# Kernel optimization log

Measured on AMD Instinct MI355X. Metric: run time of the kernel, lower is better.

## Reference

```python
import jax, jax.numpy as jnp
import numpy as np

B_GRAPHS = 64
N_PER = 2048          # nodes per graph (uniform -> total = B*N)
D = 256               # hidden_dim
U = D // 2            # GRU units per direction
L_LAYERS = 2


def setup_inputs() -> dict:
    key = jax.random.key(0)
    ks = jax.random.split(key, 8)
    T = B_GRAPHS * N_PER
    states = jax.random.normal(ks[0], (T, D), dtype=jnp.float32)
    rng = np.random.default_rng(0)
    pos = np.zeros((B_GRAPHS, N_PER), dtype=np.int32)
    for g in range(B_GRAPHS):
        mask = rng.random(N_PER) < 0.5
        L = int(mask.sum())
        pos[g, mask] = rng.permutation(L).astype(np.int32) + 1
    node_positions = jnp.asarray(pos.reshape(-1))
    graph_sizes = jnp.full((B_GRAPHS,), N_PER, dtype=jnp.int32)
    # GRU params (Keras GRU reset_after=True): kernel [D,3u], recurrent [u,3u], bias [2,3u]
    def mk(k):
        k1, k2, k3 = jax.random.split(k, 3)
        K = jax.random.normal(k1, (L_LAYERS, D, 3 * U), dtype=jnp.float32) * 0.06
        R = jax.random.normal(k2, (L_LAYERS, U, 3 * U), dtype=jnp.float32) * 0.06
        b = jax.random.normal(k3, (L_LAYERS, 2, 3 * U), dtype=jnp.float32) * 0.02
        return K, R, b
    K_fwd, R_fwd, b_fwd = mk(ks[1])
    K_bwd, R_bwd, b_bwd = mk(ks[2])
    return {"states": states, "node_positions": node_positions,
            "graph_sizes": graph_sizes, "training": 0,
            "K_fwd": K_fwd, "R_fwd": R_fwd, "b_fwd": b_fwd,
            "K_bwd": K_bwd, "R_bwd": R_bwd, "b_bwd": b_bwd}


def _gru_dir(seq, mask, K, R, b, reverse):
    # seq [B,S,Din], mask [B,S] -> outputs [B,S,U] (Keras GRU, reset_after=True)
    xs = jnp.swapaxes(seq, 0, 1)                 # [S,B,Din]
    ms = jnp.swapaxes(mask, 0, 1)                # [S,B]
    x_proj = xs @ K + b[0]                       # [S,B,3U] input projections
    Bsz = seq.shape[0]
    h0 = jnp.zeros((Bsz, U), seq.dtype)
    def step(h, inp):
        xp, m = inp
        hp = h @ R + b[1]                        # [B,3U]
        xz, xr, xh = jnp.split(xp, 3, axis=-1)
        hz, hr, hh = jnp.split(hp, 3, axis=-1)
        z = jax.nn.sigmoid(xz + hz)
        r = jax.nn.sigmoid(xr + hr)
        cand = jnp.tanh(xh + r * hh)
        h_new = z * h + (1.0 - z) * cand
        h = jnp.where(m[:, None], h_new, h)      # padded steps carry state
        return h, h
    _, ys = jax.lax.scan(step, h0, (x_proj, ms), reverse=reverse)
    return jnp.swapaxes(ys, 0, 1)


def _forward(states, node_positions, graph_sizes, training,
             K_fwd, R_fwd, b_fwd, K_bwd, R_bwd, b_bwd):
    T = states.shape[0]
    B = graph_sizes.shape[0]
    S = T // B  # max leaf-seq length (uniform graph sizes; bounds leaf count)
    gid = jnp.repeat(jnp.arange(B, dtype=jnp.int32), graph_sizes,
                     total_repeat_length=T)                      # [T]
    leaf = node_positions != 0                                   # [T]
    pos0 = node_positions - 1                                    # valid where leaf
    slot = jnp.where(leaf, pos0, S)                              # dump non-leaves
    # Pack ragged leaf sequences into dense [B,S,D] (extra slot S = trash)
    seq = jnp.zeros((B, S + 1, D), states.dtype).at[gid, slot].set(states)[:, :S]
    smask = jnp.zeros((B, S + 1), bool).at[gid, slot].set(leaf)[:, :S]
    drop_rate = 0.1 * float(training)
    x = seq
    key = jax.random.key(42)
    for l in range(L_LAYERS):
        yf = _gru_dir(x, smask, K_fwd[l], R_fwd[l], b_fwd[l], reverse=False)
        yb = _gru_dir(x, smask, K_bwd[l], R_bwd[l], b_bwd[l], reverse=True)
        x = jnp.concatenate([yf, yb], axis=-1)                   # [B,S,D]
        if drop_rate > 0.0:
            key, sub = jax.random.split(key)
            keep = jax.random.bernoulli(sub, 1.0 - drop_rate, x.shape)
            x = jnp.where(keep, x / (1.0 - drop_rate), 0.0)
    # Unpack: leaf nodes get RNN output, non-leaves keep original state
    gathered = x[gid, jnp.clip(pos0, 0)]                         # [T,D]
    return jnp.where(leaf[:, None], gathered, states)


def reference(states, node_positions, graph_sizes, training,
              K_fwd, R_fwd, b_fwd, K_bwd, R_bwd, b_bwd):
    return _forward(states, node_positions, graph_sizes, training,
                    K_fwd, R_fwd, b_fwd, K_bwd, R_bwd, b_bwd)
```

## Files before the change

kernel.cpp:

```cpp
#include <hip/hip_runtime.h>
#include <hip/hip_bf16.h>

#define B_GRAPHS 64
#define NPER     2048
#define T_NODES  (B_GRAPHS*NPER)
#define D_DIM    256
#define U_DIM    128
#define TU       384
#define XPW      768

typedef unsigned short ushortT;
typedef unsigned int   uint32;

typedef __attribute__((ext_vector_type(4))) float  f32x4;
typedef __attribute__((ext_vector_type(8))) __bf16 bf16x8;
typedef _Float16 f16;
typedef __attribute__((ext_vector_type(2))) _Float16 f16x2;

static __device__ __forceinline__ ushortT f2bf(float f) {
  union { float f; uint32 u; } a; a.f = f;
  uint32 u = a.u;
  return (ushortT)((u + 0x7fffu + ((u >> 16) & 1u)) >> 16);
}
static __device__ __forceinline__ float bf2f(ushortT h) {
  union { uint32 u; float f; } a; a.u = ((uint32)h) << 16; return a.f;
}
static __device__ __forceinline__ f16x2 u2h(uint32 u) {
  union { uint32 u; f16x2 h; } x; x.u = u; return x.h;
}
static __device__ __forceinline__ float dot2f(f16x2 a, f16x2 b, float c) {
#if __has_builtin(__builtin_amdgcn_fdot2)
  return __builtin_amdgcn_fdot2(a, b, c, false);
#else
  return c + (float)a.x * (float)b.x + (float)a.y * (float)b.y;
#endif
}

__global__ __launch_bounds__(256) void prep_kernel(
    const float* __restrict__ Kf, const float* __restrict__ Kb,
    const float* __restrict__ bfw, const float* __restrict__ bbw,
    ushortT* __restrict__ Wt, float* __restrict__ b0)
{
  int idx = blockIdx.x * 256 + threadIdx.x;
  if (idx < 2 * XPW * D_DIM) {
    int l = idx / (XPW * D_DIM);
    int rem = idx % (XPW * D_DIM);
    int c = rem / D_DIM, k = rem % D_DIM;
    float v = (c < TU) ? Kf[(size_t)l * D_DIM * TU + (size_t)k * TU + c]
                       : Kb[(size_t)l * D_DIM * TU + (size_t)k * TU + (c - TU)];
    Wt[idx] = f2bf(v);
  } else {
    int i2 = idx - 2 * XPW * D_DIM;
    if (i2 < 2 * XPW) {
      int l = i2 / XPW, c = i2 % XPW;
      b0[i2] = (c < TU) ? bfw[l * 2 * TU + c] : bbw[l * 2 * TU + (c - TU)];
    }
  }
}

__global__ __launch_bounds__(256) void nodeofL_kernel(
    const int* __restrict__ pos, int* __restrict__ nodeof, int* __restrict__ L)
{
  int g = blockIdx.x, tid = threadIdx.x;
  __shared__ int red[256];
  int cnt = 0;
  for (int i = 0; i < NPER / 256; ++i) {
    int t = g * NPER + i * 256 + tid;
    int p = pos[t];
    if (p) { nodeof[g * NPER + p - 1] = t; cnt++; }
  }
  red[tid] = cnt; __syncthreads();
  for (int s = 128; s > 0; s >>= 1) {
    if (tid < s) red[tid] += red[tid + s];
    __syncthreads();
  }
  if (tid == 0) L[g] = red[0];
}

#if __has_builtin(__builtin_amdgcn_global_load_lds)
#define GLD_LDS(gsrc, ldst) \
  __builtin_amdgcn_global_load_lds((const __attribute__((address_space(1))) void*)(gsrc), \
                                   (__attribute__((address_space(3))) void*)(ldst), 16, 0, 0)
#define HAVE_GLD_LDS 1
#else
#define HAVE_GLD_LDS 0
#endif

__global__ __launch_bounds__(256) void gemm_kernel(
    const float* __restrict__ statesA, const ushortT* __restrict__ Adense,
    const ushortT* __restrict__ Wt, const float* __restrict__ b0,
    const int* __restrict__ nodeof, const int* __restrict__ L,
    ushortT* __restrict__ xp, int layer, int mode)
{
  int mblk = blockIdx.x, nblk = blockIdx.y;
  int g = mblk >> 4;
  int sBase = (mblk & 15) << 7;
  int Lg = L[g];
  if (sBase >= Lg) return;

  __shared__ __align__(16) ushortT As[128 * 32];
  __shared__ __align__(16) ushortT Bs[128 * 32];

  int tid = threadIdx.x;
  int lane = tid & 63, wid = tid >> 6;
  int wr = wid >> 1, wc = wid & 1;
  f32x4 acc[4][4];
  for (int i = 0; i < 4; i++) for (int n = 0; n < 4; n++) acc[i][n] = (f32x4){0.f,0.f,0.f,0.f};

  for (int kb = 0; kb < 8; ++kb) {
    __syncthreads();
    for (int c = 0; c < 2; ++c) {
      int flat = c * 4096 + tid * 16;
      int col = flat >> 6;
      size_t srcB = ((size_t)(layer * XPW + nblk * 128 + col)) * 512 + kb * 64 + (flat & 63);
#if HAVE_GLD_LDS
      GLD_LDS((const char*)Wt + srcB, (char*)Bs + c * 4096 + wid * 1024);
#else
      *(uint4*)((char*)Bs + flat) = *(const uint4*)((const char*)Wt + srcB);
#endif
    }
    if (mode) {
      for (int c = 0; c < 2; ++c) {
        int flat = c * 4096 + tid * 16;
        int row = flat >> 6;
        size_t srcA = ((size_t)(mblk * 128 + row)) * 512 + kb * 64 + (flat & 63);
#if HAVE_GLD_LDS
        GLD_LDS((const char*)Adense + srcA, (char*)As + c * 4096 + wid * 1024);
#else
        *(uint4*)((char*)As + flat) = *(const uint4*)((const char*)Adense + srcA);
#endif
      }
    } else {
      for (int c = 0; c < 2; ++c) {
        int flat = c * 4096 + tid * 16;
        int row = flat >> 6;
        int s = sBase + row;
        if (s < Lg) {
          int nt = nodeof[g * NPER + s];
          const float* sp = statesA + (size_t)nt * D_DIM + kb * 32 + ((flat & 63) >> 1);
          float4 u0 = *(const float4*)sp;
          float4 u1 = *(const float4*)(sp + 4);
          union { ushortT us[8]; uint4 v; } pk;
          pk.us[0] = f2bf(u0.x); pk.us[1] = f2bf(u0.y); pk.us[2] = f2bf(u0.z); pk.us[3] = f2bf(u0.w);
          pk.us[4] = f2bf(u1.x); pk.us[5] = f2bf(u1.y); pk.us[6] = f2bf(u1.z); pk.us[7] = f2bf(u1.w);
          *(uint4*)((char*)As + flat) = pk.v;
        }
      }
    }
    __syncthreads();

    bf16x8 af[4], bfr[4];
    for (int i = 0; i < 4; i++) {
      int off = (wr * 64 + i * 16 + (lane & 15)) * 32 + (lane >> 4) * 8;
      af[i] = *(const bf16x8*)&As[off];
    }
    for (int n = 0; n < 4; n++) {
      int off = (wc * 64 + n * 16 + (lane & 15)) * 32 + (lane >> 4) * 8;
      bfr[n] = *(const bf16x8*)&Bs[off];
    }
    for (int i = 0; i < 4; i++)
      for (int n = 0; n < 4; n++)
        acc[i][n] = __builtin_amdgcn_mfma_f32_16x16x32_bf16(af[i], bfr[n], acc[i][n], 0, 0, 0);
  }

  for (int n = 0; n < 4; n++) {
    int gcol = nblk * 128 + wc * 64 + n * 16 + (lane & 15);
    float bb = b0[layer * XPW + gcol];
    for (int i = 0; i < 4; i++) {
      int rowBase = mblk * 128 + wr * 64 + i * 16 + (lane >> 4) * 4;
      for (int v = 0; v < 4; v++)
        xp[(size_t)(rowBase + v) * XPW + gcol] = f2bf(acc[i][n][v] + bb);
    }
  }
}

__global__ __launch_bounds__(768) void rec_kernel(
    const ushortT* __restrict__ xp,
    const float* __restrict__ Rf, const float* __restrict__ Rb,
    const float* __restrict__ bfw, const float* __restrict__ bbw,
    const int* __restrict__ L, ushortT* __restrict__ y, int layer)
{
  int g = blockIdx.x, dir = blockIdx.y;
  int Lg = L[g];
  if (Lg == 0) return;
  int tid = threadIdx.x;
  int col = tid % TU;
  int khalf = tid / TU;

  __shared__ __align__(16) f16 hpk[128];
  __shared__ float hp[768];

  const float* R = (dir ? Rb : Rf) + (size_t)layer * U_DIM * TU;
  f16x2 rr[32];
  #pragma unroll
  for (int m = 0; m < 32; ++m) {
    int k = khalf * 64 + 2 * m;
    f16x2 p;
    p.x = (f16)R[(size_t)k * TU + col];
    p.y = (f16)R[(size_t)(k + 1) * TU + col];
    rr[m] = p;
  }
  float b1col = (dir ? bbw : bfw)[layer * 2 * TU + TU + col];
  float accInit = khalf ? 0.0f : b1col;

  if (tid < 128) hpk[tid] = (f16)0.0f;
  float hreg = 0.0f;
  __syncthreads();

  int j = tid;
  ushortT xzu = 0, xru = 0, xhu = 0;
  size_t xbase = (size_t)g * NPER * XPW + (size_t)dir * TU;
  if (tid < 128) {
    int pos = dir ? (Lg - 1) : 0;
    const ushortT* p = xp + xbase + (size_t)pos * XPW + j;
    xzu = p[0]; xru = p[128]; xhu = p[256];
  }

  for (int s = 0; s < Lg; ++s) {
    float a0 = accInit, a1 = 0.0f;
    const uint4* hv = (const uint4*)&hpk[khalf * 64];
    #pragma unroll
    for (int m4 = 0; m4 < 8; ++m4) {
      uint4 q = hv[m4];
      a0 = dot2f(u2h(q.x), rr[4 * m4 + 0], a0);
      a1 = dot2f(u2h(q.y), rr[4 * m4 + 1], a1);
      a0 = dot2f(u2h(q.z), rr[4 * m4 + 2], a0);
      a1 = dot2f(u2h(q.w), rr[4 * m4 + 3], a1);
    }
    hp[tid] = a0 + a1;
    __syncthreads();

    if (tid < 128) {
      int pos = dir ? (Lg - 1 - s) : s;
      float hz = hp[j]       + hp[TU + j];
      float hr = hp[128 + j] + hp[TU + 128 + j];
      float hh = hp[256 + j] + hp[TU + 256 + j];
      float xz = bf2f(xzu), xr = bf2f(xru), xh = bf2f(xhu);
      float z = 1.0f / (1.0f + __expf(-(xz + hz)));
      float r = 1.0f / (1.0f + __expf(-(xr + hr)));
      float ch = xh + r * hh;
      float e = __expf(2.0f * fabsf(ch));
      float th = 1.0f - 2.0f / (e + 1.0f);
      float cand = (ch >= 0.0f) ? th : -th;
      float hnew = z * hreg + (1.0f - z) * cand;
      hreg = hnew;
      hpk[j] = (f16)hnew;
      y[(size_t)(g * NPER + pos) * D_DIM + dir * U_DIM + j] = f2bf(hnew);
      int s2 = s + 1;
      if (s2 < Lg) {
        int pos2 = dir ? (Lg - 1 - s2) : s2;
        const ushortT* p = xp + xbase + (size_t)pos2 * XPW + j;
        xzu = p[0]; xru = p[128]; xhu = p[256];
      }
    }
    __syncthreads();
  }
}

__global__ __launch_bounds__(256) void unpack_kernel(
    const float* __restrict__ states, const int* __restrict__ pos,
    const ushortT* __restrict__ y, float* __restrict__ out)
{
  int node = blockIdx.x * 4 + (threadIdx.x >> 6);
  int lane = threadIdx.x & 63;
  int p = pos[node];
  int g = node >> 11;
  float4 v;
  if (p) {
    const ushortT* yp = y + (size_t)(g * NPER + p - 1) * D_DIM + lane * 4;
    v = make_float4(bf2f(yp[0]), bf2f(yp[1]), bf2f(yp[2]), bf2f(yp[3]));
  } else {
    v = *(const float4*)(states + (size_t)node * D_DIM + lane * 4);
  }
  *(float4*)(out + (size_t)node * D_DIM + lane * 4) = v;
}

extern "C" void kernel_launch(void* const* d_in, const int* in_sizes, int n_in,
                              void* d_out, int out_size, void* d_ws, size_t ws_size,
                              hipStream_t stream) {
  const float* states = (const float*)d_in[0];
  const int*   pos    = (const int*)d_in[1];
  const float* Kf  = (const float*)d_in[4];
  const float* Rf  = (const float*)d_in[5];
  const float* bfw = (const float*)d_in[6];
  const float* Kb  = (const float*)d_in[7];
  const float* Rb  = (const float*)d_in[8];
  const float* bbw = (const float*)d_in[9];

  char* ws = (char*)d_ws;
  int*     L      = (int*)(ws + 0);
  int*     nodeof = (int*)(ws + 256);
  ushortT* Wt     = (ushortT*)(ws + 524544);
  float*   b0     = (float*)(ws + 1310976);
  ushortT* xp     = (ushortT*)(ws + 1317120);
  ushortT* y      = (ushortT*)(ws + 202643712);

  prep_kernel<<<1542, 256, 0, stream>>>(Kf, Kb, bfw, bbw, Wt, b0);
  nodeofL_kernel<<<64, 256, 0, stream>>>(pos, nodeof, L);

  dim3 ggrid(1024, 6);
  dim3 rgrid(64, 2);

  gemm_kernel<<<ggrid, 256, 0, stream>>>(states, (const ushortT*)nullptr, Wt, b0, nodeof, L, xp, 0, 0);
  rec_kernel<<<rgrid, 768, 0, stream>>>(xp, Rf, Rb, bfw, bbw, L, y, 0);
  gemm_kernel<<<ggrid, 256, 0, stream>>>(states, y, Wt, b0, nodeof, L, xp, 1, 1);
  rec_kernel<<<rgrid, 768, 0, stream>>>(xp, Rf, Rb, bfw, bbw, L, y, 1);

  unpack_kernel<<<32768, 256, 0, stream>>>(states, pos, y, (float*)d_out);
}
```

Before: 1.529 ms.

## Restructure GRU recurrence to one barrier per step with double-buffered hidden state

The recurrent kernel drops from 768 to 256 threads. Each lane now computes all three gates for one unit over half of K, and the two halves are combined with a cross-lane shuffle instead of a shared-memory partial-sum array. The hidden state is double-buffered in LDS, so each step needs only one barrier instead of two. The xp inputs are prefetched two steps ahead, and divisions use hardware reciprocals. The gains come from a shorter serial critical path per time step, at the cost of three times more register-held weights per thread (96 packed f16 pairs) and slightly lower-precision reciprocals.

```diff
diff --git a/kernel.cpp b/kernel.cpp
--- a/kernel.cpp
+++ b/kernel.cpp
@@ -33,6 +33,13 @@
   return __builtin_amdgcn_fdot2(a, b, c, false);
 #else
   return c + (float)a.x * (float)b.x + (float)a.y * (float)b.y;
+#endif
+}
+static __device__ __forceinline__ float rcpf(float x) {
+#if __has_builtin(__builtin_amdgcn_rcpf)
+  return __builtin_amdgcn_rcpf(x);
+#else
+  return 1.0f / x;
 #endif
 }
 
@@ -174,7 +181,7 @@
   }
 }
 
-__global__ __launch_bounds__(768) void rec_kernel(
+__global__ __launch_bounds__(256) void rec_kernel(
     const ushortT* __restrict__ xp,
     const float* __restrict__ Rf, const float* __restrict__ Rb,
     const float* __restrict__ bfw, const float* __restrict__ bbw,
@@ -184,77 +191,104 @@
   int Lg = L[g];
   if (Lg == 0) return;
   int tid = threadIdx.x;
-  int col = tid % TU;
-  int khalf = tid / TU;
-
-  __shared__ __align__(16) f16 hpk[128];
-  __shared__ float hp[768];
-
-  const float* R = (dir ? Rb : Rf) + (size_t)layer * U_DIM * TU;
-  f16x2 rr[32];
+  int wave = tid >> 6, lane = tid & 63;
+  int jl = lane & 31, half = lane >> 5;
+  int j = wave * 32 + jl;
+
+  __shared__ __align__(16) f16 hpk[2][128];
+
+  const float* R  = (dir ? Rb : Rf) + (size_t)layer * U_DIM * TU;
+  const float* b1 = (dir ? bbw : bfw) + layer * 2 * TU + TU;
+
+  f16x2 rz[32], rg[32], rh[32];
   #pragma unroll
   for (int m = 0; m < 32; ++m) {
-    int k = khalf * 64 + 2 * m;
-    f16x2 p;
-    p.x = (f16)R[(size_t)k * TU + col];
-    p.y = (f16)R[(size_t)(k + 1) * TU + col];
-    rr[m] = p;
-  }
-  float b1col = (dir ? bbw : bfw)[layer * 2 * TU + TU + col];
-  float accInit = khalf ? 0.0f : b1col;
-
-  if (tid < 128) hpk[tid] = (f16)0.0f;
+    int k = half * 64 + 2 * m;
+    const float* p0 = R + (size_t)k * TU;
+    const float* p1 = p0 + TU;
+    f16x2 a, b, c;
+    a.x = (f16)p0[j];        a.y = (f16)p1[j];
+    b.x = (f16)p0[128 + j];  b.y = (f16)p1[128 + j];
+    c.x = (f16)p0[256 + j];  c.y = (f16)p1[256 + j];
+    rz[m] = a; rg[m] = b; rh[m] = c;
+  }
+  float bz = half ? 0.0f : b1[j];
+  float br = half ? 0.0f : b1[128 + j];
+  float bh = half ? 0.0f : b1[256 + j];
+
+  if (tid < 128) hpk[0][tid] = (f16)0.0f;
   float hreg = 0.0f;
   __syncthreads();
 
-  int j = tid;
-  ushortT xzu = 0, xru = 0, xhu = 0;
   size_t xbase = (size_t)g * NPER * XPW + (size_t)dir * TU;
-  if (tid < 128) {
-    int pos = dir ? (Lg - 1) : 0;
-    const ushortT* p = xp + xbase + (size_t)pos * XPW + j;
-    xzu = p[0]; xru = p[128]; xhu = p[256];
-  }
-
-  for (int s = 0; s < Lg; ++s) {
-    float a0 = accInit, a1 = 0.0f;
-    const uint4* hv = (const uint4*)&hpk[khalf * 64];
-    #pragma unroll
-    for (int m4 = 0; m4 < 8; ++m4) {
-      uint4 q = hv[m4];
-      a0 = dot2f(u2h(q.x), rr[4 * m4 + 0], a0);
-      a1 = dot2f(u2h(q.y), rr[4 * m4 + 1], a1);
-      a0 = dot2f(u2h(q.z), rr[4 * m4 + 2], a0);
-      a1 = dot2f(u2h(q.w), rr[4 * m4 + 3], a1);
-    }
-    hp[tid] = a0 + a1;
-    __syncthreads();
-
-    if (tid < 128) {
-      int pos = dir ? (Lg - 1 - s) : s;
-      float hz = hp[j]       + hp[TU + j];
-      float hr = hp[128 + j] + hp[TU + 128 + j];
-      float hh = hp[256 + j] + hp[TU + 256 + j];
-      float xz = bf2f(xzu), xr = bf2f(xru), xh = bf2f(xhu);
-      float z = 1.0f / (1.0f + __expf(-(xz + hz)));
-      float r = 1.0f / (1.0f + __expf(-(xr + hr)));
-      float ch = xh + r * hh;
-      float e = __expf(2.0f * fabsf(ch));
-      float th = 1.0f - 2.0f / (e + 1.0f);
-      float cand = (ch >= 0.0f) ? th : -th;
-      float hnew = z * hreg + (1.0f - z) * cand;
-      hreg = hnew;
-      hpk[j] = (f16)hnew;
-      y[(size_t)(g * NPER + pos) * D_DIM + dir * U_DIM + j] = f2bf(hnew);
-      int s2 = s + 1;
-      if (s2 < Lg) {
-        int pos2 = dir ? (Lg - 1 - s2) : s2;
-        const ushortT* p = xp + xbase + (size_t)pos2 * XPW + j;
-        xzu = p[0]; xru = p[128]; xhu = p[256];
-      }
-    }
-    __syncthreads();
-  }
+  ushortT xzA = 0, xrA = 0, xhA = 0, xzB = 0, xrB = 0, xhB = 0;
+  {
+    int p0 = dir ? (Lg - 1) : 0;
+    const ushortT* p = xp + xbase + (size_t)p0 * XPW;
+    xzA = p[j]; xrA = p[128 + j]; xhA = p[256 + j];
+    if (Lg > 1) {
+      int p1 = dir ? (Lg - 2) : 1;
+      const ushortT* q = xp + xbase + (size_t)p1 * XPW;
+      xzB = q[j]; xrB = q[128 + j]; xhB = q[256 + j];
+    }
+  }
+
+#define GRU_STEP(P, XZ, XR, XH, SS)                                              \
+  {                                                                              \
+    const int s_ = (SS);                                                         \
+    float xzf = bf2f(XZ), xrf = bf2f(XR), xhf = bf2f(XH);                        \
+    const int sp_ = s_ + 2;                                                      \
+    if (sp_ < Lg) {                                                              \
+      int pos2 = dir ? (Lg - 1 - sp_) : sp_;                                     \
+      const ushortT* p_ = xp + xbase + (size_t)pos2 * XPW;                       \
+      XZ = p_[j]; XR = p_[128 + j]; XH = p_[256 + j];                            \
+    }                                                                            \
+    const uint4* hv = (const uint4*)&hpk[P][half * 64];                          \
+    uint32 hw[32];                                                               \
+    _Pragma("unroll")                                                            \
+    for (int q8 = 0; q8 < 8; ++q8) {                                             \
+      uint4 v_ = hv[q8];                                                         \
+      hw[4*q8] = v_.x; hw[4*q8+1] = v_.y; hw[4*q8+2] = v_.z; hw[4*q8+3] = v_.w;  \
+    }                                                                            \
+    float az0 = bz, ar0 = br, ah0 = bh, az1 = 0.f, ar1 = 0.f, ah1 = 0.f;         \
+    _Pragma("unroll")                                                            \
+    for (int m = 0; m < 32; m += 2) {                                            \
+      az0 = dot2f(u2h(hw[m]),   rz[m],   az0);                                   \
+      ar0 = dot2f(u2h(hw[m]),   rg[m],   ar0);                                   \
+      ah0 = dot2f(u2h(hw[m]),   rh[m],   ah0);                                   \
+      az1 = dot2f(u2h(hw[m+1]), rz[m+1], az1);                                   \
+      ar1 = dot2f(u2h(hw[m+1]), rg[m+1], ar1);                                   \
+      ah1 = dot2f(u2h(hw[m+1]), rh[m+1], ah1);                                   \
+    }                                                                            \
+    float hz = az0 + az1, hr = ar0 + ar1, hh = ah0 + ah1;                        \
+    hz += __shfl_xor(hz, 32);                                                    \
+    hr += __shfl_xor(hr, 32);                                                    \
+    hh += __shfl_xor(hh, 32);                                                    \
+    float z = rcpf(1.0f + __expf(-(xzf + hz)));                                  \
+    float r = rcpf(1.0f + __expf(-(xrf + hr)));                                  \
+    float ch = xhf + r * hh;                                                     \
+    float e = __expf(2.0f * __builtin_fabsf(ch));                                \
+    float th = 1.0f - 2.0f * rcpf(e + 1.0f);                                     \
+    float cand = __builtin_copysignf(th, ch);                                    \
+    float hnew = cand + z * (hreg - cand);                                       \
+    hreg = hnew;                                                                 \
+    if (half) {                                                                  \
+      int pos_ = dir ? (Lg - 1 - s_) : s_;                                       \
+      y[(size_t)(g * NPER + pos_) * D_DIM + dir * U_DIM + j] = f2bf(hnew);       \
+    } else {                                                                     \
+      hpk[(P) ^ 1][j] = (f16)hnew;                                               \
+    }                                                                            \
+    asm volatile("s_waitcnt lgkmcnt(0)" ::: "memory");                           \
+    __builtin_amdgcn_sched_barrier(0);                                           \
+    __builtin_amdgcn_s_barrier();                                                \
+    __builtin_amdgcn_sched_barrier(0);                                           \
+  }
+
+  for (int s = 0; s < Lg; s += 2) {
+    GRU_STEP(0, xzA, xrA, xhA, s);
+    if (s + 1 < Lg) GRU_STEP(1, xzB, xrB, xhB, s + 1);
+  }
+#undef GRU_STEP
 }
 
 __global__ __launch_bounds__(256) void unpack_kernel(
@@ -302,9 +336,9 @@
   dim3 rgrid(64, 2);
 
   gemm_kernel<<<ggrid, 256, 0, stream>>>(states, (const ushortT*)nullptr, Wt, b0, nodeof, L, xp, 0, 0);
-  rec_kernel<<<rgrid, 768, 0, stream>>>(xp, Rf, Rb, bfw, bbw, L, y, 0);
+  rec_kernel<<<rgrid, 256, 0, stream>>>(xp, Rf, Rb, bfw, bbw, L, y, 0);
   gemm_kernel<<<ggrid, 256, 0, stream>>>(states, y, Wt, b0, nodeof, L, xp, 1, 1);
-  rec_kernel<<<rgrid, 768, 0, stream>>>(xp, Rf, Rb, bfw, bbw, L, y, 1);
+  rec_kernel<<<rgrid, 256, 0, stream>>>(xp, Rf, Rb, bfw, bbw, L, y, 1);
 
   unpack_kernel<<<32768, 256, 0, stream>>>(states, pos, y, (float*)d_out);
 }
```

Measured after the change: 1.298 ms. -15.1%, faster.

## Batch 16 graphs per block in GRU recurrence using f16 MFMA

Applied to the files above, without the earlier changes.

The recurrent kernel now processes 16 graphs per block, one block per direction per group of 16. It computes h@R for all 16 at once with 16x16x32 f16 MFMA instructions, holding the weights in registers and keeping double-buffered, swizzled hidden states in LDS. Each timestep needs one barrier instead of two and drops the separate LDS partial-sum reduction. The log2(e) and 2·log2(e) factors are folded into the input weights, biases and recurrent weights, so the gates can use hardware exp2 and rcp. The trade-offs: only 8 blocks run, each group steps for the longest graph in it, and precision shifts to f16 MFMA with approximate transcendentals.

```diff
diff --git a/kernel.cpp b/kernel.cpp
--- a/kernel.cpp
+++ b/kernel.cpp
@@ -15,7 +15,10 @@
 typedef __attribute__((ext_vector_type(4))) float  f32x4;
 typedef __attribute__((ext_vector_type(8))) __bf16 bf16x8;
 typedef _Float16 f16;
-typedef __attribute__((ext_vector_type(2))) _Float16 f16x2;
+typedef __attribute__((ext_vector_type(8))) _Float16 f16x8;
+
+#define GAS __attribute__((address_space(1)))
+#define LOG2E_F 1.4426950408889634f
 
 static __device__ __forceinline__ ushortT f2bf(float f) {
   union { float f; uint32 u; } a; a.f = f;
@@ -25,15 +28,25 @@
 static __device__ __forceinline__ float bf2f(ushortT h) {
   union { uint32 u; float f; } a; a.u = ((uint32)h) << 16; return a.f;
 }
-static __device__ __forceinline__ f16x2 u2h(uint32 u) {
-  union { uint32 u; f16x2 h; } x; x.u = u; return x.h;
-}
-static __device__ __forceinline__ float dot2f(f16x2 a, f16x2 b, float c) {
-#if __has_builtin(__builtin_amdgcn_fdot2)
-  return __builtin_amdgcn_fdot2(a, b, c, false);
-#else
-  return c + (float)a.x * (float)b.x + (float)a.y * (float)b.y;
-#endif
+static __device__ __forceinline__ float rcpf(float x) {
+#if __has_builtin(__builtin_amdgcn_rcpf)
+  return __builtin_amdgcn_rcpf(x);
+#else
+  return 1.0f / x;
+#endif
+}
+static __device__ __forceinline__ float exp2f_hw(float x) {
+#if __has_builtin(__builtin_amdgcn_exp2f)
+  return __builtin_amdgcn_exp2f(x);
+#else
+  return __expf(0.69314718055994531f * x);
+#endif
+}
+static __device__ __forceinline__ ushortT gload_u16(const ushortT* p) {
+  return *(const GAS ushortT*)p;
+}
+static __device__ __forceinline__ void gstore_u16(ushortT* p, ushortT v) {
+  *(GAS ushortT*)p = v;
 }
 
 __global__ __launch_bounds__(256) void prep_kernel(
@@ -48,12 +61,15 @@
     int c = rem / D_DIM, k = rem % D_DIM;
     float v = (c < TU) ? Kf[(size_t)l * D_DIM * TU + (size_t)k * TU + c]
                        : Kb[(size_t)l * D_DIM * TU + (size_t)k * TU + (c - TU)];
-    Wt[idx] = f2bf(v);
+    float sc = ((c % TU) < 256) ? LOG2E_F : 2.0f * LOG2E_F;
+    Wt[idx] = f2bf(v * sc);
   } else {
     int i2 = idx - 2 * XPW * D_DIM;
     if (i2 < 2 * XPW) {
       int l = i2 / XPW, c = i2 % XPW;
-      b0[i2] = (c < TU) ? bfw[l * 2 * TU + c] : bbw[l * 2 * TU + (c - TU)];
+      float v = (c < TU) ? bfw[l * 2 * TU + c] : bbw[l * 2 * TU + (c - TU)];
+      float sc = ((c % TU) < 256) ? LOG2E_F : 2.0f * LOG2E_F;
+      b0[i2] = v * sc;
     }
   }
 }
@@ -79,7 +95,7 @@
 
 #if __has_builtin(__builtin_amdgcn_global_load_lds)
 #define GLD_LDS(gsrc, ldst) \
-  __builtin_amdgcn_global_load_lds((const __attribute__((address_space(1))) void*)(gsrc), \
+  __builtin_amdgcn_global_load_lds((const GAS void*)(gsrc), \
                                    (__attribute__((address_space(3))) void*)(ldst), 16, 0, 0)
 #define HAVE_GLD_LDS 1
 #else
@@ -174,86 +190,136 @@
   }
 }
 
-__global__ __launch_bounds__(768) void rec_kernel(
+__global__ __launch_bounds__(512) void rec_kernel(
     const ushortT* __restrict__ xp,
     const float* __restrict__ Rf, const float* __restrict__ Rb,
     const float* __restrict__ bfw, const float* __restrict__ bbw,
     const int* __restrict__ L, ushortT* __restrict__ y, int layer)
 {
-  int g = blockIdx.x, dir = blockIdx.y;
-  int Lg = L[g];
-  if (Lg == 0) return;
+  int dir = blockIdx.y;
+  int g0 = blockIdx.x * 16;
   int tid = threadIdx.x;
-  int col = tid % TU;
-  int khalf = tid / TU;
-
-  __shared__ __align__(16) f16 hpk[128];
-  __shared__ float hp[768];
-
-  const float* R = (dir ? Rb : Rf) + (size_t)layer * U_DIM * TU;
-  f16x2 rr[32];
-  #pragma unroll
-  for (int m = 0; m < 32; ++m) {
-    int k = khalf * 64 + 2 * m;
-    f16x2 p;
-    p.x = (f16)R[(size_t)k * TU + col];
-    p.y = (f16)R[(size_t)(k + 1) * TU + col];
-    rr[m] = p;
-  }
-  float b1col = (dir ? bbw : bfw)[layer * 2 * TU + TU + col];
-  float accInit = khalf ? 0.0f : b1col;
-
-  if (tid < 128) hpk[tid] = (f16)0.0f;
-  float hreg = 0.0f;
+  int wave = tid >> 6, lane = tid & 63;
+  int jc = lane & 15;
+  int qa = lane >> 4;
+  int ut = wave;
+  int j  = ut * 16 + jc;
+
+  __shared__ __align__(16) ushortT Hb[2][16 * 128];
+
+  int Lmax = 0;
+  #pragma unroll 1
+  for (int i = 0; i < 16; ++i) { int t = L[g0 + i]; Lmax = t > Lmax ? t : Lmax; }
+  if (Lmax == 0) return;
+  int Lg4[4];
+  #pragma unroll
+  for (int v = 0; v < 4; ++v) Lg4[v] = L[g0 + qa * 4 + v];
+
+  const float* Rsrc = (dir ? Rb : Rf) + (size_t)layer * U_DIM * TU;
+  const float* b1p  = (dir ? bbw : bfw) + layer * 2 * TU + TU;
+
+  f16x8 bw[3][4];
+  float b1s[3];
+  #pragma unroll
+  for (int gate = 0; gate < 3; ++gate) {
+    float sc = (gate < 2) ? LOG2E_F : 2.0f * LOG2E_F;
+    int col = gate * 128 + j;
+    b1s[gate] = b1p[col] * sc;
+    #pragma unroll
+    for (int q = 0; q < 4; ++q) {
+      union { f16 h[8]; f16x8 v; } pk;
+      #pragma unroll
+      for (int e = 0; e < 8; ++e) {
+        int k = q * 32 + qa * 8 + e;
+        pk.h[e] = (f16)(Rsrc[(size_t)k * TU + col] * sc);
+      }
+      bw[gate][q] = pk.v;
+    }
+  }
+
+  for (int i = tid; i < 16 * 128; i += 512) { Hb[0][i] = 0; Hb[1][i] = 0; }
+  float hold[4] = {0.f, 0.f, 0.f, 0.f};
   __syncthreads();
 
-  int j = tid;
-  ushortT xzu = 0, xru = 0, xhu = 0;
-  size_t xbase = (size_t)g * NPER * XPW + (size_t)dir * TU;
-  if (tid < 128) {
-    int pos = dir ? (Lg - 1) : 0;
-    const ushortT* p = xp + xbase + (size_t)pos * XPW + j;
-    xzu = p[0]; xru = p[128]; xhu = p[256];
-  }
-
-  for (int s = 0; s < Lg; ++s) {
-    float a0 = accInit, a1 = 0.0f;
-    const uint4* hv = (const uint4*)&hpk[khalf * 64];
-    #pragma unroll
-    for (int m4 = 0; m4 < 8; ++m4) {
-      uint4 q = hv[m4];
-      a0 = dot2f(u2h(q.x), rr[4 * m4 + 0], a0);
-      a1 = dot2f(u2h(q.y), rr[4 * m4 + 1], a1);
-      a0 = dot2f(u2h(q.z), rr[4 * m4 + 2], a0);
-      a1 = dot2f(u2h(q.w), rr[4 * m4 + 3], a1);
-    }
-    hp[tid] = a0 + a1;
-    __syncthreads();
-
-    if (tid < 128) {
-      int pos = dir ? (Lg - 1 - s) : s;
-      float hz = hp[j]       + hp[TU + j];
-      float hr = hp[128 + j] + hp[TU + 128 + j];
-      float hh = hp[256 + j] + hp[TU + 256 + j];
-      float xz = bf2f(xzu), xr = bf2f(xru), xh = bf2f(xhu);
-      float z = 1.0f / (1.0f + __expf(-(xz + hz)));
-      float r = 1.0f / (1.0f + __expf(-(xr + hr)));
-      float ch = xh + r * hh;
-      float e = __expf(2.0f * fabsf(ch));
-      float th = 1.0f - 2.0f / (e + 1.0f);
-      float cand = (ch >= 0.0f) ? th : -th;
-      float hnew = z * hreg + (1.0f - z) * cand;
-      hreg = hnew;
-      hpk[j] = (f16)hnew;
-      y[(size_t)(g * NPER + pos) * D_DIM + dir * U_DIM + j] = f2bf(hnew);
-      int s2 = s + 1;
-      if (s2 < Lg) {
-        int pos2 = dir ? (Lg - 1 - s2) : s2;
-        const ushortT* p = xp + xbase + (size_t)pos2 * XPW + j;
-        xzu = p[0]; xru = p[128]; xhu = p[256];
-      }
-    }
-    __syncthreads();
+  const ushortT* xptr[4];
+  ushortT* yptr[4];
+  #pragma unroll
+  for (int v = 0; v < 4; ++v) {
+    int c = qa * 4 + v;
+    int Lg = Lg4[v];
+    int pos0 = dir ? (Lg > 0 ? Lg - 1 : 0) : 0;
+    xptr[v] = xp + ((size_t)(g0 + c) * NPER + pos0) * XPW + dir * TU + j;
+    yptr[v] = y  + ((size_t)(g0 + c) * NPER + pos0) * D_DIM + dir * U_DIM + j;
+  }
+  const int xstep = dir ? -XPW : XPW;
+  const int ystep = dir ? -D_DIM : D_DIM;
+
+  ushortT xu[12];
+  #pragma unroll
+  for (int v = 0; v < 4; ++v) {
+    xu[v*3+0] = gload_u16(xptr[v]);
+    xu[v*3+1] = gload_u16(xptr[v] + 128);
+    xu[v*3+2] = gload_u16(xptr[v] + 256);
+  }
+
+  const int abase = jc * 256 + qa * 16;
+  const int aswz  = (jc & 7) << 4;
+  const int cw    = qa * 4;
+  int wb4[4];
+  #pragma unroll
+  for (int v = 0; v < 4; ++v) {
+    int c = cw + v;
+    wb4[v] = (c * 256 + j * 2) ^ ((c & 7) << 4);
+  }
+
+  for (int s = 0; s < Lmax; ++s) {
+    char* Hrd = (char*)Hb[s & 1];
+    char* Hwr = (char*)Hb[(s & 1) ^ 1];
+    f16x8 afr[4];
+    #pragma unroll
+    for (int q = 0; q < 4; ++q)
+      afr[q] = *(const f16x8*)(Hrd + ((abase + q * 64) ^ aswz));
+    float xf[12];
+    #pragma unroll
+    for (int i = 0; i < 12; ++i) xf[i] = bf2f(xu[i]);
+    #pragma unroll
+    for (int v = 0; v < 4; ++v) {
+      xptr[v] += xstep;
+      xu[v*3+0] = gload_u16(xptr[v]);
+      xu[v*3+1] = gload_u16(xptr[v] + 128);
+      xu[v*3+2] = gload_u16(xptr[v] + 256);
+    }
+    f32x4 accz = {0.f,0.f,0.f,0.f}, accr = {0.f,0.f,0.f,0.f}, acch = {0.f,0.f,0.f,0.f};
+    #pragma unroll
+    for (int q = 0; q < 4; ++q) {
+      accz = __builtin_amdgcn_mfma_f32_16x16x32_f16(afr[q], bw[0][q], accz, 0, 0, 0);
+      accr = __builtin_amdgcn_mfma_f32_16x16x32_f16(afr[q], bw[1][q], accr, 0, 0, 0);
+      acch = __builtin_amdgcn_mfma_f32_16x16x32_f16(afr[q], bw[2][q], acch, 0, 0, 0);
+    }
+    #pragma unroll
+    for (int v = 0; v < 4; ++v) {
+      float hz = accz[v] + b1s[0];
+      float hr = accr[v] + b1s[1];
+      float hh = acch[v] + b1s[2];
+      float z = rcpf(1.0f + exp2f_hw(-(xf[v*3+0] + hz)));
+      float r = rcpf(1.0f + exp2f_hw(-(xf[v*3+1] + hr)));
+      float a = xf[v*3+2] + r * hh;
+      float e = exp2f_hw(__builtin_fabsf(a));
+      float th = 1.0f - 2.0f * rcpf(e + 1.0f);
+      float cand = __builtin_copysignf(th, a);
+      float hnew = cand + z * (hold[v] - cand);
+      bool live = s < Lg4[v];
+      float hst = live ? hnew : hold[v];
+      hold[v] = hst;
+      if (live) gstore_u16(yptr[v], f2bf(hst));
+      yptr[v] += ystep;
+      f16 hph = (f16)hst;
+      *(ushortT*)(Hwr + wb4[v]) = __builtin_bit_cast(ushortT, hph);
+    }
+    asm volatile("s_waitcnt lgkmcnt(0)" ::: "memory");
+    __builtin_amdgcn_sched_barrier(0);
+    __builtin_amdgcn_s_barrier();
+    __builtin_amdgcn_sched_barrier(0);
   }
 }
 
@@ -299,12 +365,12 @@
   nodeofL_kernel<<<64, 256, 0, stream>>>(pos, nodeof, L);
 
   dim3 ggrid(1024, 6);
-  dim3 rgrid(64, 2);
+  dim3 rgrid(4, 2);
 
   gemm_kernel<<<ggrid, 256, 0, stream>>>(states, (const ushortT*)nullptr, Wt, b0, nodeof, L, xp, 0, 0);
-  rec_kernel<<<rgrid, 768, 0, stream>>>(xp, Rf, Rb, bfw, bbw, L, y, 0);
+  rec_kernel<<<rgrid, 512, 0, stream>>>(xp, Rf, Rb, bfw, bbw, L, y, 0);
   gemm_kernel<<<ggrid, 256, 0, stream>>>(states, y, Wt, b0, nodeof, L, xp, 1, 1);
-  rec_kernel<<<rgrid, 768, 0, stream>>>(xp, Rf, Rb, bfw, bbw, L, y, 1);
+  rec_kernel<<<rgrid, 512, 0, stream>>>(xp, Rf, Rb, bfw, bbw, L, y, 1);
 
   unpack_kernel<<<32768, 256, 0, stream>>>(states, pos, y, (float*)d_out);
 }
```

Measured after the change: 2.085 ms. 1.36x slower.
